# Kernel optimization log

Measured on AMD Instinct MI355X. Metric: run time of the kernel, lower is better.

Reference implementation:

```python
import jax, jax.numpy as jnp
import numpy as np

B, N, D = 16, 4096, 6
NUM_CENTERS, K = 1024, 32
EPS = 1e-5


def setup_inputs() -> dict:
    key = jax.random.key(0)
    ks = jax.random.split(key, 6)
    xyz = jax.random.uniform(ks[0], (B, N, 3), dtype=jnp.float32)
    features = jax.random.normal(ks[1], (B, N, D), dtype=jnp.float32)
    W1 = jax.random.normal(ks[2], (3 + D, 64), dtype=jnp.float32) * 0.1
    W2 = jax.random.normal(ks[3], (64, 64), dtype=jnp.float32) * 0.1
    W3 = jax.random.normal(ks[4], (64, 128), dtype=jnp.float32) * 0.1
    return {
        "xyz": xyz, "features": features,
        "W1": W1, "g1": jnp.ones((64,)), "b1": jnp.zeros((64,)),
        "W2": W2, "g2": jnp.ones((64,)), "b2": jnp.zeros((64,)),
        "W3": W3, "g3": jnp.ones((128,)), "b3": jnp.zeros((128,)),
    }


def square_distance(a, b):
    # a: [B,S,3], b: [B,N,3] -> [B,S,N] squared euclidean distance
    d2 = (jnp.sum(a * a, -1)[:, :, None]
          + jnp.sum(b * b, -1)[:, None, :]
          - 2.0 * jnp.einsum('bsc,bnc->bsn', a, b))
    return jnp.maximum(d2, 0.0)


def farthest_point_sample(xyz, num_centers):
    # xyz: [B,N,3] -> centers_idx: [B,S]. First center fixed at index 0
    # (original uses a random first index; deterministic here).
    Bn = xyz.shape[0]
    batch = jnp.arange(Bn)
    first = jnp.zeros((Bn,), jnp.int32)
    d0 = jnp.sum((xyz - xyz[batch, first][:, None, :]) ** 2, -1)  # [B,N]

    def step(dist_closest, _):
        idx = jnp.argmax(dist_closest, axis=1).astype(jnp.int32)  # [B]
        c = xyz[batch, idx]                                        # [B,3]
        d = jnp.sum((xyz - c[:, None, :]) ** 2, -1)                # [B,N]
        return jnp.minimum(dist_closest, d), idx

    _, rest = jax.lax.scan(step, d0, None, length=num_centers - 1)  # [S-1,B]
    return jnp.concatenate([first[:, None], rest.T], axis=1)        # [B,S]


def gather_bsk(points, idx):
    # points: [B,N,C], idx: [B,S,K] -> [B,S,K,C]
    Bn = points.shape[0]
    return points[jnp.arange(Bn)[:, None, None], idx]


def conv_bn_relu(x, W, g, b):
    # 1x1 conv (channel matmul) + training-mode BatchNorm (biased var) + ReLU
    x = jnp.einsum('bskc,co->bsko', x, W)
    m = jnp.mean(x, axis=(0, 1, 2))
    v = jnp.var(x, axis=(0, 1, 2))
    return jax.nn.relu((x - m) * jax.lax.rsqrt(v + EPS) * g + b)


def reference(xyz, features, W1, g1, b1, W2, g2, b2, W3, g3, b3):
    Bn = xyz.shape[0]
    batch = jnp.arange(Bn)
    centers_idx = farthest_point_sample(xyz, NUM_CENTERS)          # [B,S]
    centers_xyz = xyz[batch[:, None], centers_idx]                  # [B,S,3]

    # kNN grouping: [B,S,N] distance matrix, top-K smallest
    d2 = square_distance(centers_xyz, xyz)
    _, group_idx = jax.lax.top_k(-d2, K)                            # [B,S,K]

    group_xyz = gather_bsk(xyz, group_idx) - centers_xyz[:, :, None, :]
    group_feat = gather_bsk(features, group_idx)
    group = jnp.concatenate([group_xyz, group_feat], axis=-1)       # [B,S,K,3+D]

    x = conv_bn_relu(group, W1, g1, b1)
    x = conv_bn_relu(x, W2, g2, b2)
    x = conv_bn_relu(x, W3, g3, b3)
    centers_features = jnp.max(x, axis=2)                           # [B,S,C_out]
    return centers_xyz, centers_features
```

## Files before the change

### kernel.cpp

```cpp
#include <hip/hip_runtime.h>

#define BN_   16
#define NPTS  4096
#define DFEAT 6
#define SCTR  1024
#define KNN   32
#define RTOT  (BN_*SCTR*KNN)
#define EPSV  1e-5f
#define RNF   524288.0f
#define NREP  64

__device__ __forceinline__ float fmulx(float a, float b){ return __fmul_rn(a,b); }
__device__ __forceinline__ float faddx(float a, float b){ return __fadd_rn(a,b); }
__device__ __forceinline__ float fsubx(float a, float b){ return __fsub_rn(a,b); }
__device__ __forceinline__ float sq3x(float x, float y, float z){
  return faddx(faddx(fmulx(x,x), fmulx(y,y)), fmulx(z,z));
}
__device__ __forceinline__ float dot3fma(float ax, float ay, float az,
                                         float bx, float by, float bz){
  return __fmaf_rn(az, bz, __fmaf_rn(ay, by, __fmul_rn(ax, bx)));
}

__device__ __forceinline__ unsigned fkey(float f){
  unsigned u = __float_as_uint(f);
  return (u & 0x80000000u) ? ~u : (u | 0x80000000u);
}
__device__ __forceinline__ float funkey(unsigned k){
  return (k & 0x80000000u) ? __uint_as_float(k & 0x7fffffffu) : __uint_as_float(~k);
}

template<int CTRL>
__device__ __forceinline__ unsigned dpp_mv(unsigned v){
  return (unsigned)__builtin_amdgcn_update_dpp((int)v, (int)v, CTRL, 0xf, 0xf, false);
}
__device__ __forceinline__ unsigned wave_umax_b(unsigned v){
  unsigned o;
  o=dpp_mv<0x111>(v); v=v>o?v:o;
  o=dpp_mv<0x112>(v); v=v>o?v:o;
  o=dpp_mv<0x114>(v); v=v>o?v:o;
  o=dpp_mv<0x118>(v); v=v>o?v:o;
  o=dpp_mv<0x142>(v); v=v>o?v:o;
  o=dpp_mv<0x143>(v); v=v>o?v:o;
  return (unsigned)__builtin_amdgcn_readlane((int)v, 63);
}
__device__ __forceinline__ unsigned wave_umin_b(unsigned v){
  unsigned o;
  o=dpp_mv<0x111>(v); v=v<o?v:o;
  o=dpp_mv<0x112>(v); v=v<o?v:o;
  o=dpp_mv<0x114>(v); v=v<o?v:o;
  o=dpp_mv<0x118>(v); v=v<o?v:o;
  o=dpp_mv<0x142>(v); v=v<o?v:o;
  o=dpp_mv<0x143>(v); v=v<o?v:o;
  return (unsigned)__builtin_amdgcn_readlane((int)v, 63);
}

__global__ __launch_bounds__(256) void k_fps(const float* __restrict__ xyz,
                                             float* __restrict__ cxyz){
  const int b = blockIdx.x, tid = threadIdx.x;
  const int wave = tid>>6, lane = tid&63;
  const float* X = xyz + (size_t)b*NPTS*3;
  __shared__ float Xl[NPTS*3];
  __shared__ float Cl[SCTR*3];
  __shared__ unsigned long long slot[2][4];
  for(int i=tid;i<NPTS*3;i+=256) Xl[i]=X[i];
  __syncthreads();
  float px[16],py[16],pz[16],mind[16];
  const float c0x=Xl[0], c0y=Xl[1], c0z=Xl[2];
#pragma unroll
  for(int t=0;t<16;t++){
    const int j = lane + 64*(wave*16+t);
    px[t]=Xl[j*3]; py[t]=Xl[j*3+1]; pz[t]=Xl[j*3+2];
    mind[t]=sq3x(fsubx(px[t],c0x), fsubx(py[t],c0y), fsubx(pz[t],c0z));
  }
  if(tid==0){ Cl[0]=c0x; Cl[1]=c0y; Cl[2]=c0z; }
  float bv=-1.0f; int bj=0x7fffffff;
#pragma unroll
  for(int t=0;t<16;t++){
    const int j = lane + 64*(wave*16+t);
    if(mind[t]>bv){ bv=mind[t]; bj=j; }
  }
  for(int it=1; it<SCTR; ++it){
    const unsigned uv = __float_as_uint(bv);
    const unsigned M  = wave_umax_b(uv);
    const unsigned nj = (uv == M) ? ~(unsigned)bj : 0u;
    const unsigned NJ = wave_umax_b(nj);
    if(lane==0) slot[it&1][wave] = ((unsigned long long)M<<32) | NJ;
    __syncthreads();
    unsigned long long k0=slot[it&1][0], k1=slot[it&1][1],
                       k2=slot[it&1][2], k3=slot[it&1][3];
    unsigned long long ka = k0>k1?k0:k1;
    unsigned long long kb = k2>k3?k2:k3;
    unsigned long long kw = ka>kb?ka:kb;
    const int w = (int)(~(unsigned)kw);
    const float cx=Xl[w*3], cy=Xl[w*3+1], cz=Xl[w*3+2];
    if(tid==0){ Cl[it*3]=cx; Cl[it*3+1]=cy; Cl[it*3+2]=cz; }
    bv=-1.0f; bj=0x7fffffff;
#pragma unroll
    for(int t=0;t<16;t++){
      float d = sq3x(fsubx(px[t],cx), fsubx(py[t],cy), fsubx(pz[t],cz));
      float nm = fminf(mind[t], d);
      mind[t]=nm;
      const int j = lane + 64*(wave*16+t);
      if(nm>bv){ bv=nm; bj=j; }
    }
  }
  __syncthreads();
  float* O = cxyz + (size_t)b*SCTR*3;
  for(int i=tid;i<SCTR*3;i+=256) O[i]=Cl[i];
}

__global__ __launch_bounds__(256) void k_select(const float* __restrict__ xyz,
                                                const float* __restrict__ cxyz,
                                                int* __restrict__ gidx){
  const int lane = threadIdx.x & 63;
  const int cid  = blockIdx.x*4 + (threadIdx.x>>6);
  const int b = cid>>10;
  const float* X = xyz + (size_t)b*NPTS*3;
  const float* C = cxyz + (size_t)cid*3;
  const float cx=C[0], cy=C[1], cz=C[2];
  const float a2 = sq3x(cx,cy,cz);
  float d[64];
#pragma unroll
  for(int t=0;t<64;t++){
    int j = lane + (t<<6);
    float x=X[j*3], y=X[j*3+1], z=X[j*3+2];
    float b2 = sq3x(x,y,z);
    float dt = dot3fma(cx,cy,cz, x,y,z);
    float dd = fsubx(faddx(a2,b2), fmulx(2.0f,dt));
    d[t] = fmaxf(dd, 0.0f);
  }
  float q0v=3.0e38f, q1v=3.0e38f, q2v=3.0e38f, q3v=3.0e38f;
  int   q0t=0, q1t=16, q2t=32, q3t=48;
#pragma unroll
  for(int k=0;k<16;k++){ if(d[k]    < q0v){ q0v=d[k];    q0t=k;    } }
#pragma unroll
  for(int k=0;k<16;k++){ if(d[16+k] < q1v){ q1v=d[16+k]; q1t=16+k; } }
#pragma unroll
  for(int k=0;k<16;k++){ if(d[32+k] < q2v){ q2v=d[32+k]; q2t=32+k; } }
#pragma unroll
  for(int k=0;k<16;k++){ if(d[48+k] < q3v){ q3v=d[48+k]; q3t=48+k; } }
  unsigned long long taken = 0ull;
  int* out = gidx + (size_t)cid*KNN;
#pragma unroll 1
  for(int r=0;r<KNN;r++){
    float mv = q0v; int mt = q0t;
    if(q1v < mv){ mv=q1v; mt=q1t; }
    if(q2v < mv){ mv=q2v; mt=q2t; }
    if(q3v < mv){ mv=q3v; mt=q3t; }
    const unsigned um = __float_as_uint(mv);
    const unsigned Mw = wave_umin_b(um);
    const unsigned jc = (um == Mw) ? (unsigned)(lane + (mt<<6)) : 0xffffffffu;
    const unsigned WJ = wave_umin_b(jc);
    const int wl = (int)(WJ & 63u);
    const int wt = (int)(WJ >> 6);
    if(lane == wl){
      out[r] = (int)WJ;
      taken |= (1ull << wt);
    }
    const int wq = wt >> 4;
#define RESCAN_Q(QV,QT,BASE) \
    if(lane == wl){ \
      float nv=3.0e38f; int nt=BASE; \
      _Pragma("unroll") \
      for(int k2=0;k2<16;k2++){ \
        if(!(taken & (1ull<<(BASE+k2))) && d[BASE+k2] < nv){ nv=d[BASE+k2]; nt=BASE+k2; } \
      } \
      QV=nv; QT=nt; \
    }
    if(wq==0)      { RESCAN_Q(q0v,q0t,0)  }
    else if(wq==1) { RESCAN_Q(q1v,q1t,16) }
    else if(wq==2) { RESCAN_Q(q2v,q2t,32) }
    else           { RESCAN_Q(q3v,q3t,48) }
#undef RESCAN_Q
  }
}

__device__ __forceinline__ void stage_in(float* INt, int rbase,
                                         const float* __restrict__ xyz,
                                         const float* __restrict__ feat,
                                         const float* __restrict__ cxyz,
                                         const int* __restrict__ gidx){
  const int tid = threadIdx.x;
  const int row = tid>>2, sub = tid&3;
  const int r  = rbase + row;
  const int bb = r>>15, ss=(r>>5)&1023;
  const int idx = gidx[r];
  if(sub==0){
    const float* P = xyz  + ((size_t)bb*NPTS + idx)*3;
    const float* C = cxyz + ((size_t)(bb*SCTR)+ss)*3;
    INt[0*68+row] = P[0]-C[0];
    INt[1*68+row] = P[1]-C[1];
    INt[2*68+row] = P[2]-C[2];
  }else{
    const float* F = feat + ((size_t)bb*NPTS + idx)*6;
    const int c = (sub-1)*2;
    INt[(3+c)*68+row] = F[c];
    INt[(4+c)*68+row] = F[c+1];
  }
}

__device__ __forceinline__ void gemm1(const float* INt, const float* __restrict__ W1,
                                      int rt, int ct, float acc[4][4]){
#pragma unroll
  for(int i=0;i<4;i++)
#pragma unroll
    for(int j=0;j<4;j++) acc[i][j]=0.f;
#pragma unroll
  for(int c=0;c<9;c++){
    const float4 a = *(const float4*)&INt[c*68 + rt*4];
    const float4 w = *(const float4*)&W1[c*64 + ct*4];
    const float av[4]={a.x,a.y,a.z,a.w}, wv[4]={w.x,w.y,w.z,w.w};
#pragma unroll
    for(int i=0;i<4;i++)
#pragma unroll
      for(int j=0;j<4;j++) acc[i][j] += av[i]*wv[j];
  }
}

__device__ __forceinline__ float fold_rep(const float* __restrict__ pstats, int off){
  float s=0.f;
#pragma unroll 8
  for(int c=0;c<NREP;c++) s += pstats[c*512 + off];
  return s;
}

__global__ __launch_bounds__(64) void k_coef(const float* __restrict__ pstats,
                                             const float* __restrict__ g,
                                             const float* __restrict__ b,
                                             float* __restrict__ coefo,
                                             int off){
  const int t = threadIdx.x;
  float sm = fold_rep(pstats, off+t);
  float sq = fold_rep(pstats, off+64+t);
  float m  = sm/RNF;
  float vv = sq/RNF - m*m;
  float A  = rsqrtf(vv+EPSV)*g[t];
  coefo[t]    = A;
  coefo[64+t] = b[t]-m*A;
}

__global__ __launch_bounds__(256) void k_stats1(const float* __restrict__ xyz,
                                                const float* __restrict__ feat,
                                                const float* __restrict__ cxyz,
                                                const int* __restrict__ gidx,
                                                const float* __restrict__ W1,
                                                float* __restrict__ pstats){
  __shared__ __align__(16) float INt[9*68];
  __shared__ float sb[64], qb[64];
  const int tid=threadIdx.x;
  if(tid<64){ sb[tid]=0.f; qb[tid]=0.f; }
  const int rt=tid&15, ct=tid>>4;
  float s0=0.f,s1=0.f,s2=0.f,s3=0.f, p0=0.f,p1=0.f,p2=0.f,p3=0.f;
#pragma unroll 1
  for(int h=0;h<4;h++){
    if(h) __syncthreads();
    stage_in(INt, blockIdx.x*256 + h*64, xyz, feat, cxyz, gidx);
    __syncthreads();
    float acc[4][4];
    gemm1(INt, W1, rt, ct, acc);
    {
      float s=0.f,q=0.f;
#pragma unroll
      for(int i=0;i<4;i++){ float v=acc[i][0]; s+=v; q+=v*v; }
      s0+=s; p0+=q;
    }
    {
      float s=0.f,q=0.f;
#pragma unroll
      for(int i=0;i<4;i++){ float v=acc[i][1]; s+=v; q+=v*v; }
      s1+=s; p1+=q;
    }
    {
      float s=0.f,q=0.f;
#pragma unroll
      for(int i=0;i<4;i++){ float v=acc[i][2]; s+=v; q+=v*v; }
      s2+=s; p2+=q;
    }
    {
      float s=0.f,q=0.f;
#pragma unroll
      for(int i=0;i<4;i++){ float v=acc[i][3]; s+=v; q+=v*v; }
      s3+=s; p3+=q;
    }
  }
  atomicAdd(&sb[ct*4+0], s0); atomicAdd(&qb[ct*4+0], p0);
  atomicAdd(&sb[ct*4+1], s1); atomicAdd(&qb[ct*4+1], p1);
  atomicAdd(&sb[ct*4+2], s2); atomicAdd(&qb[ct*4+2], p2);
  atomicAdd(&sb[ct*4+3], s3); atomicAdd(&qb[ct*4+3], p3);
  __syncthreads();
  if(tid<64){
    float* ps = pstats + (size_t)(blockIdx.x & (NREP-1))*512;
    atomicAdd(&ps[tid], sb[tid]); atomicAdd(&ps[64+tid], qb[tid]);
  }
}

template<bool WRITEZ>
__device__ __forceinline__ void stats2_body(const float* xyz, const float* feat,
                                            const float* cxyz, const int* gidx,
                                            const float* W1,
                                            const float* __restrict__ coef,
                                            const float* __restrict__ W2,
                                            float* pstats, float* Z2){
  __shared__ __align__(16) float INt[9*68];
  __shared__ __align__(16) float A1t[64*68];
  __shared__ float af1A[64], af1B[64];
  __shared__ float sb[64], qb[64];
  const int tid=threadIdx.x;
  if(tid<64){
    af1A[tid]=coef[tid]; af1B[tid]=coef[64+tid];
    sb[tid]=0.f; qb[tid]=0.f;
  }
  const int rt=tid&15, ct=tid>>4;
  float s0=0.f,s1=0.f,s2=0.f,s3=0.f, p0=0.f,p1=0.f,p2=0.f,p3=0.f;
#pragma unroll 1
  for(int h=0;h<4;h++){
    if(h) __syncthreads();
    stage_in(INt, blockIdx.x*256 + h*64, xyz, feat, cxyz, gidx);
    __syncthreads();
    float acc1[4][4];
    gemm1(INt, W1, rt, ct, acc1);
#pragma unroll
    for(int j=0;j<4;j++){
      const int o=ct*4+j; const float A=af1A[o], Bc=af1B[o];
#pragma unroll
      for(int i=0;i<4;i++) A1t[o*68 + rt*4+i] = fmaxf(acc1[i][j]*A+Bc, 0.f);
    }
    __syncthreads();
    float acc2[4][4];
#pragma unroll
    for(int i=0;i<4;i++)
#pragma unroll
      for(int j=0;j<4;j++) acc2[i][j]=0.f;
#pragma unroll
    for(int c=0;c<64;c++){
      const float4 a = *(const float4*)&A1t[c*68 + rt*4];
      const float4 w = *(const float4*)&W2[c*64 + ct*4];
      const float av[4]={a.x,a.y,a.z,a.w}, wv[4]={w.x,w.y,w.z,w.w};
#pragma unroll
      for(int i=0;i<4;i++)
#pragma unroll
        for(int j=0;j<4;j++) acc2[i][j] += av[i]*wv[j];
    }
    if(WRITEZ){
#pragma unroll
      for(int i=0;i<4;i++){
        float4 v = make_float4(acc2[i][0],acc2[i][1],acc2[i][2],acc2[i][3]);
        *(float4*)&Z2[((size_t)(blockIdx.x*4+h)*64 + rt*4+i)*64 + ct*4] = v;
      }
    }
    {
      float s=0.f,q=0.f;
#pragma unroll
      for(int i=0;i<4;i++){ float v=acc2[i][0]; s+=v; q+=v*v; }
      s0+=s; p0+=q;
    }
    {
      float s=0.f,q=0.f;
#pragma unroll
      for(int i=0;i<4;i++){ float v=acc2[i][1]; s+=v; q+=v*v; }
      s1+=s; p1+=q;
    }
    {
      float s=0.f,q=0.f;
#pragma unroll
      for(int i=0;i<4;i++){ float v=acc2[i][2]; s+=v; q+=v*v; }
      s2+=s; p2+=q;
    }
    {
      float s=0.f,q=0.f;
#pragma unroll
      for(int i=0;i<4;i++){ float v=acc2[i][3]; s+=v; q+=v*v; }
      s3+=s; p3+=q;
    }
  }
  atomicAdd(&sb[ct*4+0], s0); atomicAdd(&qb[ct*4+0], p0);
  atomicAdd(&sb[ct*4+1], s1); atomicAdd(&qb[ct*4+1], p1);
  atomicAdd(&sb[ct*4+2], s2); atomicAdd(&qb[ct*4+2], p2);
  atomicAdd(&sb[ct*4+3], s3); atomicAdd(&qb[ct*4+3], p3);
  __syncthreads();
  if(tid<64){
    float* ps = pstats + (size_t)(blockIdx.x & (NREP-1))*512;
    atomicAdd(&ps[128+tid], sb[tid]); atomicAdd(&ps[192+tid], qb[tid]);
  }
}

__global__ __launch_bounds__(256) void k_stats2(const float* __restrict__ xyz,
                                                const float* __restrict__ feat,
                                                const float* __restrict__ cxyz,
                                                const int* __restrict__ gidx,
                                                const float* __restrict__ W1,
                                                const float* __restrict__ coef,
                                                const float* __restrict__ W2,
                                                float* __restrict__ pstats){
  stats2_body<false>(xyz,feat,cxyz,gidx,W1,coef,W2,pstats,nullptr);
}
__global__ __launch_bounds__(256) void k_stats2m(const float* __restrict__ xyz,
                                                 const float* __restrict__ feat,
                                                 const float* __restrict__ cxyz,
                                                 const int* __restrict__ gidx,
                                                 const float* __restrict__ W1,
                                                 const float* __restrict__ coef,
                                                 const float* __restrict__ W2,
                                                 float* __restrict__ pstats,
                                                 float* __restrict__ Z2){
  stats2_body<true>(xyz,feat,cxyz,gidx,W1,coef,W2,pstats,Z2);
}

__global__ __launch_bounds__(256) void k_layer3(const float* __restrict__ xyz,
                                                const float* __restrict__ feat,
                                                const float* __restrict__ cxyz,
                                                const int* __restrict__ gidx,
                                                const float* __restrict__ W1,
                                                const float* __restrict__ coef,
                                                const float* __restrict__ W2,
                                                const float* __restrict__ W3,
                                                float* __restrict__ pstats,
                                                float* __restrict__ premax){
  __shared__ __align__(16) float INt[9*68];
  __shared__ __align__(16) float A1t[64*68];
  __shared__ float af1A[64], af1B[64], af2A[64], af2B[64];
  __shared__ unsigned mx[256];
  __shared__ float s3b[256], q3b[256];
  const int tid=threadIdx.x;
  if(tid<64){
    af1A[tid]=coef[tid];     af1B[tid]=coef[64+tid];
    af2A[tid]=coef[128+tid]; af2B[tid]=coef[192+tid];
  }
  mx[tid]=0u; s3b[tid]=0.f; q3b[tid]=0.f;
  stage_in(INt, blockIdx.x*64, xyz, feat, cxyz, gidx);
  __syncthreads();
  const int rt=tid&15, ct=tid>>4;
  float acc1[4][4];
  gemm1(INt, W1, rt, ct, acc1);
#pragma unroll
  for(int j=0;j<4;j++){
    const int o=ct*4+j; const float A=af1A[o], Bc=af1B[o];
#pragma unroll
    for(int i=0;i<4;i++) A1t[o*68 + rt*4+i] = fmaxf(acc1[i][j]*A+Bc, 0.f);
  }
  __syncthreads();
  float acc2[4][4];
#pragma unroll
  for(int i=0;i<4;i++)
#pragma unroll
    for(int j=0;j<4;j++) acc2[i][j]=0.f;
#pragma unroll
  for(int c=0;c<64;c++){
    const float4 a = *(const float4*)&A1t[c*68 + rt*4];
    const float4 w = *(const float4*)&W2[c*64 + ct*4];
    const float av[4]={a.x,a.y,a.z,a.w}, wv[4]={w.x,w.y,w.z,w.w};
#pragma unroll
    for(int i=0;i<4;i++)
#pragma unroll
      for(int j=0;j<4;j++) acc2[i][j] += av[i]*wv[j];
  }
  float a2v[4][4];
#pragma unroll
  for(int j=0;j<4;j++){
    const int o=ct*4+j; const float A=af2A[o], Bc=af2B[o];
#pragma unroll
    for(int i=0;i<4;i++) a2v[i][j]=fmaxf(acc2[i][j]*A+Bc, 0.f);
  }
  __syncthreads();
#pragma unroll
  for(int j=0;j<4;j++)
#pragma unroll
    for(int i=0;i<4;i++) A1t[(ct*4+j)*68 + rt*4+i] = a2v[i][j];
  __syncthreads();
  float acc3[4][8];
#pragma unroll
  for(int i=0;i<4;i++)
#pragma unroll
    for(int j=0;j<8;j++) acc3[i][j]=0.f;
#pragma unroll
  for(int c=0;c<64;c++){
    const float4 a  = *(const float4*)&A1t[c*68 + rt*4];
    const float4 w0 = *(const float4*)&W3[c*128 + ct*8];
    const float4 w1 = *(const float4*)&W3[c*128 + ct*8 + 4];
    const float av[4]={a.x,a.y,a.z,a.w};
    const float wv[8]={w0.x,w0.y,w0.z,w0.w,w1.x,w1.y,w1.z,w1.w};
#pragma unroll
    for(int i=0;i<4;i++)
#pragma unroll
      for(int j=0;j<8;j++) acc3[i][j] += av[i]*wv[j];
  }
  const int g = rt>>3;
#pragma unroll
  for(int j=0;j<8;j++){
    const int o=ct*8+j;
    float lm=acc3[0][j], s=0.f, q=0.f;
#pragma unroll
    for(int i=0;i<4;i++){ float v=acc3[i][j]; lm=fmaxf(lm,v); s+=v; q+=v*v; }
    atomicMax(&mx[g*128+o], fkey(lm));
    atomicAdd(&s3b[g*128+o], s);
    atomicAdd(&q3b[g*128+o], q);
  }
  __syncthreads();
  {
    const int gg=tid>>7, o=tid&127;
    const int cid = blockIdx.x*2+gg;
    premax[(size_t)cid*128+o] = funkey(mx[tid]);
  }
  if(tid<128){
    float* ps = pstats + (size_t)(blockIdx.x & (NREP-1))*512;
    atomicAdd(&ps[256+tid], s3b[tid]+s3b[128+tid]);
    atomicAdd(&ps[384+tid], q3b[tid]+q3b[128+tid]);
  }
}

__global__ __launch_bounds__(256) void k_layer3z(const float* __restrict__ Z2,
                                                 const float* __restrict__ coef,
                                                 const float* __restrict__ W3,
                                                 float* __restrict__ pstats,
                                                 float* __restrict__ premax){
  __shared__ __align__(16) float A2t[64*68];
  __shared__ __align__(16) float W3l[64*128];
  __shared__ float af2A[64], af2B[64];
  __shared__ unsigned mx[256];
  __shared__ float s3b[256], q3b[256];
  const int tid=threadIdx.x;
  if(tid<64){
    af2A[tid]=coef[128+tid]; af2B[tid]=coef[192+tid];
  }
  mx[tid]=0u; s3b[tid]=0.f; q3b[tid]=0.f;
#pragma unroll
  for(int i=0;i<8;i++){
    ((float4*)W3l)[tid + i*256] = ((const float4*)W3)[tid + i*256];
  }
  __syncthreads();
  const int rt=tid&15, ct=tid>>4;
  const int row = tid>>2, cq = (tid&3)*16;
  const int g = rt>>3;
#pragma unroll 1
  for(int h=0;h<4;h++){
    const int tile = blockIdx.x*4 + h;
    {
      const float* zr = Z2 + ((size_t)tile*64 + row)*64 + cq;
      const float4 z0 = *(const float4*)(zr);
      const float4 z1 = *(const float4*)(zr+4);
      const float4 z2 = *(const float4*)(zr+8);
      const float4 z3 = *(const float4*)(zr+12);
      const float zz[16]={z0.x,z0.y,z0.z,z0.w, z1.x,z1.y,z1.z,z1.w,
                          z2.x,z2.y,z2.z,z2.w, z3.x,z3.y,z3.z,z3.w};
#pragma unroll
      for(int u=0;u<16;u++){
        const int c = cq+u;
        A2t[c*68+row] = fmaxf(zz[u]*af2A[c]+af2B[c], 0.f);
      }
    }
    __syncthreads();
    float acc3[4][8];
#pragma unroll
    for(int i=0;i<4;i++)
#pragma unroll
      for(int j=0;j<8;j++) acc3[i][j]=0.f;
#pragma unroll
    for(int c=0;c<64;c++){
      const float4 a  = *(const float4*)&A2t[c*68 + rt*4];
      const float4 w0 = *(const float4*)&W3l[c*128 + ct*8];
      const float4 w1 = *(const float4*)&W3l[c*128 + ct*8 + 4];
      const float av[4]={a.x,a.y,a.z,a.w};
      const float wv[8]={w0.x,w0.y,w0.z,w0.w,w1.x,w1.y,w1.z,w1.w};
#pragma unroll
      for(int i=0;i<4;i++)
#pragma unroll
        for(int j=0;j<8;j++) acc3[i][j] += av[i]*wv[j];
    }
#pragma unroll
    for(int j=0;j<8;j++){
      const int o=ct*8+j;
      float lm=acc3[0][j], s=0.f, q=0.f;
#pragma unroll
      for(int i=0;i<4;i++){ float v=acc3[i][j]; lm=fmaxf(lm,v); s+=v; q+=v*v; }
      atomicMax(&mx[g*128+o], fkey(lm));
      atomicAdd(&s3b[g*128+o], s);
      atomicAdd(&q3b[g*128+o], q);
    }
    __syncthreads();
    {
      const int gg=tid>>7, o=tid&127;
      const int cid = tile*2+gg;
      premax[(size_t)cid*128+o] = funkey(mx[tid]);
      mx[tid]=0u;
    }
  }
  if(tid<128){
    float* ps = pstats + (size_t)(blockIdx.x & (NREP-1))*512;
    atomicAdd(&ps[256+tid], s3b[tid]+s3b[128+tid]);
    atomicAdd(&ps[384+tid], q3b[tid]+q3b[128+tid]);
  }
}

__global__ __launch_bounds__(256) void k_red3(const float* __restrict__ pstats,
                                              float* __restrict__ cstats){
  const int t = threadIdx.x;
  cstats[t] = fold_rep(pstats, 256+t);
}

__global__ __launch_bounds__(256) void k_final(const float* __restrict__ cstats,
                                               const float* __restrict__ g3,
                                               const float* __restrict__ b3,
                                               float* __restrict__ outf){
  const int i4 = blockIdx.x*256 + threadIdx.x;
  const int o  = (i4*4) & 127;
  float4 v = *(float4*)&outf[(size_t)i4*4];
  const float r0=v.x, r1=v.y, r2=v.z, r3=v.w;
  float w0,w1,w2,w3;
  {
    float m  = cstats[o]/RNF;
    float vv = cstats[128+o]/RNF - m*m;
    float A  = rsqrtf(vv+EPSV)*g3[o];
    float Bc = b3[o]-m*A;
    w0 = fmaxf(r0*A+Bc, 0.f);
  }
  {
    float m  = cstats[o+1]/RNF;
    float vv = cstats[128+o+1]/RNF - m*m;
    float A  = rsqrtf(vv+EPSV)*g3[o+1];
    float Bc = b3[o+1]-m*A;
    w1 = fmaxf(r1*A+Bc, 0.f);
  }
  {
    float m  = cstats[o+2]/RNF;
    float vv = cstats[128+o+2]/RNF - m*m;
    float A  = rsqrtf(vv+EPSV)*g3[o+2];
    float Bc = b3[o+2]-m*A;
    w2 = fmaxf(r2*A+Bc, 0.f);
  }
  {
    float m  = cstats[o+3]/RNF;
    float vv = cstats[128+o+3]/RNF - m*m;
    float A  = rsqrtf(vv+EPSV)*g3[o+3];
    float Bc = b3[o+3]-m*A;
    w3 = fmaxf(r3*A+Bc, 0.f);
  }
  *(float4*)&outf[(size_t)i4*4] = make_float4(w0,w1,w2,w3);
}

extern "C" void kernel_launch(void* const* d_in, const int* in_sizes, int n_in,
                              void* d_out, int out_size, void* d_ws, size_t ws_size,
                              hipStream_t stream){
  const float* xyz  = (const float*)d_in[0];
  const float* feat = (const float*)d_in[1];
  const float* W1   = (const float*)d_in[2];
  const float* g1   = (const float*)d_in[3];
  const float* b1   = (const float*)d_in[4];
  const float* W2   = (const float*)d_in[5];
  const float* g2   = (const float*)d_in[6];
  const float* b2   = (const float*)d_in[7];
  const float* W3   = (const float*)d_in[8];
  const float* g3   = (const float*)d_in[9];
  const float* b3   = (const float*)d_in[10];
  float* out  = (float*)d_out;
  float* cxyz = out;
  float* outf = out + 16*1024*3;
  float* pstats = (float*)d_ws;
  float* cstats = (float*)((char*)d_ws + 131072);
  float* coef   = (float*)((char*)d_ws + 132096);
  int*   gidx   = (int*)((char*)d_ws + 133120);
  float* Z2     = (float*)((char*)d_ws + 133120 + (size_t)RTOT*4);
  const size_t need = 133120 + (size_t)RTOT*4 + (size_t)RTOT*64*4;
  const bool fast = (ws_size >= need);

  hipMemsetAsync(pstats, 0, (size_t)NREP*512*sizeof(float), stream);
  k_fps   <<<16,   256,  0, stream>>>(xyz, cxyz);
  k_select<<<4096, 256,  0, stream>>>(xyz, cxyz, gidx);
  k_stats1<<<2048, 256,  0, stream>>>(xyz, feat, cxyz, gidx, W1, pstats);
  k_coef  <<<1,    64,   0, stream>>>(pstats, g1, b1, coef, 0);
  if(fast){
    k_stats2m<<<2048, 256, 0, stream>>>(xyz, feat, cxyz, gidx, W1, coef, W2, pstats, Z2);
    k_coef  <<<1,    64,  0, stream>>>(pstats, g2, b2, coef+128, 128);
    k_layer3z<<<2048, 256, 0, stream>>>(Z2, coef, W3, pstats, outf);
  }else{
    k_stats2 <<<2048, 256, 0, stream>>>(xyz, feat, cxyz, gidx, W1, coef, W2, pstats);
    k_coef  <<<1,    64,  0, stream>>>(pstats, g2, b2, coef+128, 128);
    k_layer3 <<<8192, 256, 0, stream>>>(xyz, feat, cxyz, gidx, W1, coef, W2, W3, pstats, outf);
  }
  k_red3  <<<1,    256,  0, stream>>>(pstats, cstats);
  k_final <<<2048, 256,  0, stream>>>(cstats, g3, b3, outf);
}
```

Measured before the change: 1.394 ms.

## Fuse FPS and kNN selection into one kernel with progress-flag pipelining

Merges farthest-point sampling and kNN top-K selection into a single launch. Sixteen blocks run FPS and publish centers in chunks of 32, bumping a per-batch atomic progress counter. Another 240 persistent blocks spin on that counter and select neighbours for centers as soon as they are available, so the selection work overlaps the long serial FPS phase instead of waiting for it to finish. This relies on all blocks being co-resident to avoid deadlock, and the spinning blocks compete with FPS for resources.

```diff
diff --git a/kernel.cpp b/kernel.cpp
--- a/kernel.cpp
+++ b/kernel.cpp
@@ -9,6 +9,7 @@
 #define EPSV  1e-5f
 #define RNF   524288.0f
 #define NREP  64
+#define NSELW 240
 
 __device__ __forceinline__ float fmulx(float a, float b){ return __fmul_rn(a,b); }
 __device__ __forceinline__ float faddx(float a, float b){ return __fadd_rn(a,b); }
@@ -54,124 +55,143 @@
   return (unsigned)__builtin_amdgcn_readlane((int)v, 63);
 }
 
-__global__ __launch_bounds__(256) void k_fps(const float* __restrict__ xyz,
-                                             float* __restrict__ cxyz){
-  const int b = blockIdx.x, tid = threadIdx.x;
-  const int wave = tid>>6, lane = tid&63;
-  const float* X = xyz + (size_t)b*NPTS*3;
+__global__ __launch_bounds__(256) void k_fps_sel(const float* __restrict__ xyz,
+                                                 float* __restrict__ cxyz,
+                                                 int* __restrict__ gidx,
+                                                 int* __restrict__ progress){
   __shared__ float Xl[NPTS*3];
   __shared__ float Cl[SCTR*3];
   __shared__ unsigned long long slot[2][4];
-  for(int i=tid;i<NPTS*3;i+=256) Xl[i]=X[i];
-  __syncthreads();
-  float px[16],py[16],pz[16],mind[16];
-  const float c0x=Xl[0], c0y=Xl[1], c0z=Xl[2];
-#pragma unroll
-  for(int t=0;t<16;t++){
-    const int j = lane + 64*(wave*16+t);
-    px[t]=Xl[j*3]; py[t]=Xl[j*3+1]; pz[t]=Xl[j*3+2];
-    mind[t]=sq3x(fsubx(px[t],c0x), fsubx(py[t],c0y), fsubx(pz[t],c0z));
-  }
-  if(tid==0){ Cl[0]=c0x; Cl[1]=c0y; Cl[2]=c0z; }
-  float bv=-1.0f; int bj=0x7fffffff;
-#pragma unroll
-  for(int t=0;t<16;t++){
-    const int j = lane + 64*(wave*16+t);
-    if(mind[t]>bv){ bv=mind[t]; bj=j; }
-  }
-  for(int it=1; it<SCTR; ++it){
-    const unsigned uv = __float_as_uint(bv);
-    const unsigned M  = wave_umax_b(uv);
-    const unsigned nj = (uv == M) ? ~(unsigned)bj : 0u;
-    const unsigned NJ = wave_umax_b(nj);
-    if(lane==0) slot[it&1][wave] = ((unsigned long long)M<<32) | NJ;
+  const int tid = threadIdx.x;
+  if(blockIdx.x < 16){
+    const int b = blockIdx.x;
+    const int wave = tid>>6, lane = tid&63;
+    const float* X = xyz + (size_t)b*NPTS*3;
+    float* Ob = cxyz + (size_t)b*SCTR*3;
+    for(int i=tid;i<NPTS*3;i+=256) Xl[i]=X[i];
     __syncthreads();
-    unsigned long long k0=slot[it&1][0], k1=slot[it&1][1],
-                       k2=slot[it&1][2], k3=slot[it&1][3];
-    unsigned long long ka = k0>k1?k0:k1;
-    unsigned long long kb = k2>k3?k2:k3;
-    unsigned long long kw = ka>kb?ka:kb;
-    const int w = (int)(~(unsigned)kw);
-    const float cx=Xl[w*3], cy=Xl[w*3+1], cz=Xl[w*3+2];
-    if(tid==0){ Cl[it*3]=cx; Cl[it*3+1]=cy; Cl[it*3+2]=cz; }
-    bv=-1.0f; bj=0x7fffffff;
+    float px[16],py[16],pz[16],mind[16];
+    const float c0x=Xl[0], c0y=Xl[1], c0z=Xl[2];
 #pragma unroll
     for(int t=0;t<16;t++){
-      float d = sq3x(fsubx(px[t],cx), fsubx(py[t],cy), fsubx(pz[t],cz));
-      float nm = fminf(mind[t], d);
-      mind[t]=nm;
       const int j = lane + 64*(wave*16+t);
-      if(nm>bv){ bv=nm; bj=j; }
-    }
-  }
-  __syncthreads();
-  float* O = cxyz + (size_t)b*SCTR*3;
-  for(int i=tid;i<SCTR*3;i+=256) O[i]=Cl[i];
-}
-
-__global__ __launch_bounds__(256) void k_select(const float* __restrict__ xyz,
-                                                const float* __restrict__ cxyz,
-                                                int* __restrict__ gidx){
-  const int lane = threadIdx.x & 63;
-  const int cid  = blockIdx.x*4 + (threadIdx.x>>6);
-  const int b = cid>>10;
-  const float* X = xyz + (size_t)b*NPTS*3;
-  const float* C = cxyz + (size_t)cid*3;
-  const float cx=C[0], cy=C[1], cz=C[2];
-  const float a2 = sq3x(cx,cy,cz);
-  float d[64];
-#pragma unroll
-  for(int t=0;t<64;t++){
-    int j = lane + (t<<6);
-    float x=X[j*3], y=X[j*3+1], z=X[j*3+2];
-    float b2 = sq3x(x,y,z);
-    float dt = dot3fma(cx,cy,cz, x,y,z);
-    float dd = fsubx(faddx(a2,b2), fmulx(2.0f,dt));
-    d[t] = fmaxf(dd, 0.0f);
-  }
-  float q0v=3.0e38f, q1v=3.0e38f, q2v=3.0e38f, q3v=3.0e38f;
-  int   q0t=0, q1t=16, q2t=32, q3t=48;
-#pragma unroll
-  for(int k=0;k<16;k++){ if(d[k]    < q0v){ q0v=d[k];    q0t=k;    } }
-#pragma unroll
-  for(int k=0;k<16;k++){ if(d[16+k] < q1v){ q1v=d[16+k]; q1t=16+k; } }
-#pragma unroll
-  for(int k=0;k<16;k++){ if(d[32+k] < q2v){ q2v=d[32+k]; q2t=32+k; } }
-#pragma unroll
-  for(int k=0;k<16;k++){ if(d[48+k] < q3v){ q3v=d[48+k]; q3t=48+k; } }
-  unsigned long long taken = 0ull;
-  int* out = gidx + (size_t)cid*KNN;
+      px[t]=Xl[j*3]; py[t]=Xl[j*3+1]; pz[t]=Xl[j*3+2];
+      mind[t]=sq3x(fsubx(px[t],c0x), fsubx(py[t],c0y), fsubx(pz[t],c0z));
+    }
+    if(tid==0){ Cl[0]=c0x; Cl[1]=c0y; Cl[2]=c0z; }
+    float bv=-1.0f; int bj=0x7fffffff;
+#pragma unroll
+    for(int t=0;t<16;t++){
+      const int j = lane + 64*(wave*16+t);
+      if(mind[t]>bv){ bv=mind[t]; bj=j; }
+    }
+    for(int it=1; it<SCTR; ++it){
+      const unsigned uv = __float_as_uint(bv);
+      const unsigned M  = wave_umax_b(uv);
+      const unsigned nj = (uv == M) ? ~(unsigned)bj : 0u;
+      const unsigned NJ = wave_umax_b(nj);
+      if(lane==0) slot[it&1][wave] = ((unsigned long long)M<<32) | NJ;
+      __syncthreads();
+      unsigned long long k0=slot[it&1][0], k1=slot[it&1][1],
+                         k2=slot[it&1][2], k3=slot[it&1][3];
+      unsigned long long ka = k0>k1?k0:k1;
+      unsigned long long kb = k2>k3?k2:k3;
+      unsigned long long kw = ka>kb?ka:kb;
+      const int w = (int)(~(unsigned)kw);
+      const float cx=Xl[w*3], cy=Xl[w*3+1], cz=Xl[w*3+2];
+      if(tid==0){ Cl[it*3]=cx; Cl[it*3+1]=cy; Cl[it*3+2]=cz; }
+      bv=-1.0f; bj=0x7fffffff;
+#pragma unroll
+      for(int t=0;t<16;t++){
+        float d = sq3x(fsubx(px[t],cx), fsubx(py[t],cy), fsubx(pz[t],cz));
+        float nm = fminf(mind[t], d);
+        mind[t]=nm;
+        const int j = lane + 64*(wave*16+t);
+        if(nm>bv){ bv=nm; bj=j; }
+      }
+      if((it&31)==31){
+        __syncthreads();
+        const int base = (it>>5)*96;
+        if(tid<96) Ob[base+tid] = Cl[base+tid];
+        __syncthreads();
+        if(tid==0)
+          __hip_atomic_fetch_add(&progress[b], 32,
+                                 __ATOMIC_RELEASE, __HIP_MEMORY_SCOPE_AGENT);
+      }
+    }
+  } else {
+    const int lane = tid & 63;
+    const int wv   = tid >> 6;
+    for(int g = (int)blockIdx.x - 16; g < 4096; g += NSELW){
+      const int cid0 = g*4;
+      const int b    = cid0>>10;
+      const int need = ((cid0+3)&1023) + 1;
+      if(tid==0){
+        while(__hip_atomic_load(&progress[b],
+                                __ATOMIC_ACQUIRE, __HIP_MEMORY_SCOPE_AGENT) < need)
+          __builtin_amdgcn_s_sleep(8);
+      }
+      __syncthreads();
+      const int cid = cid0 + wv;
+      const float* X = xyz + (size_t)b*NPTS*3;
+      const float* C = cxyz + (size_t)cid*3;
+      const float cx=C[0], cy=C[1], cz=C[2];
+      const float a2 = sq3x(cx,cy,cz);
+      float d[64];
+#pragma unroll
+      for(int t=0;t<64;t++){
+        int j = lane + (t<<6);
+        float x=X[j*3], y=X[j*3+1], z=X[j*3+2];
+        float b2 = sq3x(x,y,z);
+        float dt = dot3fma(cx,cy,cz, x,y,z);
+        float dd = fsubx(faddx(a2,b2), fmulx(2.0f,dt));
+        d[t] = fmaxf(dd, 0.0f);
+      }
+      float q0v=3.0e38f, q1v=3.0e38f, q2v=3.0e38f, q3v=3.0e38f;
+      int   q0t=0, q1t=16, q2t=32, q3t=48;
+#pragma unroll
+      for(int k=0;k<16;k++){ if(d[k]    < q0v){ q0v=d[k];    q0t=k;    } }
+#pragma unroll
+      for(int k=0;k<16;k++){ if(d[16+k] < q1v){ q1v=d[16+k]; q1t=16+k; } }
+#pragma unroll
+      for(int k=0;k<16;k++){ if(d[32+k] < q2v){ q2v=d[32+k]; q2t=32+k; } }
+#pragma unroll
+      for(int k=0;k<16;k++){ if(d[48+k] < q3v){ q3v=d[48+k]; q3t=48+k; } }
+      unsigned long long taken = 0ull;
+      int* out = gidx + (size_t)cid*KNN;
 #pragma unroll 1
-  for(int r=0;r<KNN;r++){
-    float mv = q0v; int mt = q0t;
-    if(q1v < mv){ mv=q1v; mt=q1t; }
-    if(q2v < mv){ mv=q2v; mt=q2t; }
-    if(q3v < mv){ mv=q3v; mt=q3t; }
-    const unsigned um = __float_as_uint(mv);
-    const unsigned Mw = wave_umin_b(um);
-    const unsigned jc = (um == Mw) ? (unsigned)(lane + (mt<<6)) : 0xffffffffu;
-    const unsigned WJ = wave_umin_b(jc);
-    const int wl = (int)(WJ & 63u);
-    const int wt = (int)(WJ >> 6);
-    if(lane == wl){
-      out[r] = (int)WJ;
-      taken |= (1ull << wt);
-    }
-    const int wq = wt >> 4;
+      for(int r=0;r<KNN;r++){
+        float mv = q0v; int mt = q0t;
+        if(q1v < mv){ mv=q1v; mt=q1t; }
+        if(q2v < mv){ mv=q2v; mt=q2t; }
+        if(q3v < mv){ mv=q3v; mt=q3t; }
+        const unsigned um = __float_as_uint(mv);
+        const unsigned Mw = wave_umin_b(um);
+        const unsigned jc = (um == Mw) ? (unsigned)(lane + (mt<<6)) : 0xffffffffu;
+        const unsigned WJ = wave_umin_b(jc);
+        const int wl = (int)(WJ & 63u);
+        const int wt = (int)(WJ >> 6);
+        if(lane == wl){
+          out[r] = (int)WJ;
+          taken |= (1ull << wt);
+        }
+        const int wq = wt >> 4;
 #define RESCAN_Q(QV,QT,BASE) \
-    if(lane == wl){ \
-      float nv=3.0e38f; int nt=BASE; \
-      _Pragma("unroll") \
-      for(int k2=0;k2<16;k2++){ \
-        if(!(taken & (1ull<<(BASE+k2))) && d[BASE+k2] < nv){ nv=d[BASE+k2]; nt=BASE+k2; } \
-      } \
-      QV=nv; QT=nt; \
-    }
-    if(wq==0)      { RESCAN_Q(q0v,q0t,0)  }
-    else if(wq==1) { RESCAN_Q(q1v,q1t,16) }
-    else if(wq==2) { RESCAN_Q(q2v,q2t,32) }
-    else           { RESCAN_Q(q3v,q3t,48) }
+        if(lane == wl){ \
+          float nv=3.0e38f; int nt=BASE; \
+          _Pragma("unroll") \
+          for(int k2=0;k2<16;k2++){ \
+            if(!(taken & (1ull<<(BASE+k2))) && d[BASE+k2] < nv){ nv=d[BASE+k2]; nt=BASE+k2; } \
+          } \
+          QV=nv; QT=nt; \
+        }
+        if(wq==0)      { RESCAN_Q(q0v,q0t,0)  }
+        else if(wq==1) { RESCAN_Q(q1v,q1t,16) }
+        else if(wq==2) { RESCAN_Q(q2v,q2t,32) }
+        else           { RESCAN_Q(q3v,q3t,48) }
 #undef RESCAN_Q
+      }
+    }
   }
 }
 
@@ -654,17 +674,18 @@
   float* out  = (float*)d_out;
   float* cxyz = out;
   float* outf = out + 16*1024*3;
-  float* pstats = (float*)d_ws;
-  float* cstats = (float*)((char*)d_ws + 131072);
-  float* coef   = (float*)((char*)d_ws + 132096);
-  int*   gidx   = (int*)((char*)d_ws + 133120);
-  float* Z2     = (float*)((char*)d_ws + 133120 + (size_t)RTOT*4);
-  const size_t need = 133120 + (size_t)RTOT*4 + (size_t)RTOT*64*4;
+  float* pstats   = (float*)d_ws;
+  float* cstats   = (float*)((char*)d_ws + 131072);
+  float* coef     = (float*)((char*)d_ws + 132096);
+  int*   progress = (int*)  ((char*)d_ws + 133120);
+  int*   gidx     = (int*)  ((char*)d_ws + 133184);
+  float* Z2       = (float*)((char*)d_ws + 133184 + (size_t)RTOT*4);
+  const size_t need = 133184 + (size_t)RTOT*4 + (size_t)RTOT*64*4;
   const bool fast = (ws_size >= need);
 
   hipMemsetAsync(pstats, 0, (size_t)NREP*512*sizeof(float), stream);
-  k_fps   <<<16,   256,  0, stream>>>(xyz, cxyz);
-  k_select<<<4096, 256,  0, stream>>>(xyz, cxyz, gidx);
+  hipMemsetAsync(progress, 0, 16*sizeof(int), stream);
+  k_fps_sel<<<16+NSELW, 256, 0, stream>>>(xyz, cxyz, gidx, progress);
   k_stats1<<<2048, 256,  0, stream>>>(xyz, feat, cxyz, gidx, W1, pstats);
   k_coef  <<<1,    64,   0, stream>>>(pstats, g1, b1, coef, 0);
   if(fast){
```

After: 1.736 ms. 1.25x slower.
